# Performance work log

Hardware: AMD Instinct MI355X
Metric: run time of the kernel (lower is better)

Reference implementation:

```python
import jax, jax.numpy as jnp
import numpy as np

EPS = 1e-5  # BatchNorm1d default eps


def gcn_conv(x, row, col, w, n):
    # symmetric normalized aggregation: out[c] = sum_e d[row]^-1/2 d[col]^-1/2 w_e x[row]
    deg = jax.ops.segment_sum(w, col, num_segments=n)           # weighted in-degree [N]
    dinv = jnp.where(deg > 0, jax.lax.rsqrt(deg), 0.0)          # nan_to_num guard
    norm = dinv[row] * dinv[col] * w                            # [E]
    msg = x[row] * norm[:, None]                                # [E, H] gather
    return jax.ops.segment_sum(msg, col, num_segments=n)        # [N, H] scatter-add


def batchnorm(x):
    # BatchNorm1d(affine=False, track_running_stats=False): batch stats, biased var
    mu = jnp.mean(x, axis=0)
    var = jnp.mean((x - mu) ** 2, axis=0)
    return (x - mu) * jax.lax.rsqrt(var + EPS)


def setup_inputs() -> dict:
    key = jax.random.key(0)
    ks = jax.random.split(key, 7)
    N, E, D, H = 100000, 1600000, 128, 128
    x = jax.random.normal(ks[0], (N, D), dtype=jnp.float32)
    edge_index = jax.random.randint(ks[1], (2, E), 0, N, dtype=jnp.int32)
    edge_weight = jax.random.uniform(ks[2], (E,), dtype=jnp.float32)
    # xavier_uniform gain=1: limit = sqrt(6/(fan_in+fan_out))
    lim0 = float(np.sqrt(6.0 / (D + H)))
    lim1 = float(np.sqrt(6.0 / (H + H)))
    W0 = jax.random.uniform(ks[3], (H, D), dtype=jnp.float32, minval=-lim0, maxval=lim0)
    W1 = jax.random.uniform(ks[4], (H, H), dtype=jnp.float32, minval=-lim1, maxval=lim1)
    b0 = jnp.zeros((H,), jnp.float32)
    b1 = jnp.zeros((H,), jnp.float32)
    return {"x": x, "edge_index": edge_index, "edge_weight": edge_weight,
            "W0": W0, "b0": b0, "W1": W1, "b1": b1}


def reference(x, edge_index, edge_weight, W0, b0, W1, b1):
    n = x.shape[0]
    row, col = edge_index[0], edge_index[1]
    # layer 0: linear -> gcn_conv -> bias -> batchnorm -> relu
    h = x @ W0.T
    h = gcn_conv(h, row, col, edge_weight, n)
    h = jax.nn.relu(batchnorm(h + b0))
    # final layer: linear -> gcn_conv -> bias
    h = h @ W1.T
    h = gcn_conv(h, row, col, edge_weight, n)
    return h + b1
```

## Files before the change

### kernel.cpp

```cpp
#include <hip/hip_runtime.h>
#include <cstdint>
#include <cstddef>

#define EPSF 1e-5f
#define BKT 256
#define BKT_SHIFT 8
#define SC_E 4096

typedef unsigned long long ull;
typedef __attribute__((ext_vector_type(8))) short bf16x8;
typedef __attribute__((ext_vector_type(4))) float f32x4;


__global__ __launch_bounds__(512) void bucket_hist(const int* __restrict__ col,
                                                   int* __restrict__ bhist, int E, int NB) {
    __shared__ int lh[512];
    const int t = threadIdx.x;
    lh[t] = 0;
    __syncthreads();
    for (int e = blockIdx.x * 512 + t; e < E; e += gridDim.x * 512)
        atomicAdd(&lh[col[e] >> BKT_SHIFT], 1);
    __syncthreads();
    if (t < NB && lh[t]) atomicAdd(&bhist[t], lh[t]);
}

__global__ __launch_bounds__(512) void scan_buckets(const int* __restrict__ bhist,
                                                    int* __restrict__ bstart,
                                                    int* __restrict__ bcursor,
                                                    int* __restrict__ rs,
                                                    int NB, int N, int E) {
    __shared__ int part[512];
    const int t = threadIdx.x;
    part[t] = (t < NB) ? bhist[t] : 0;
    __syncthreads();
    for (int off = 1; off < 512; off <<= 1) {
        int v = (t >= off) ? part[t - off] : 0;
        __syncthreads();
        part[t] += v;
        __syncthreads();
    }
    int excl = (t == 0) ? 0 : part[t - 1];
    if (t < NB) { bstart[t] = excl; bcursor[t] = excl; }
    if (t == 0) { bstart[NB] = E; rs[N] = E; }
}

__global__ __launch_bounds__(512) void bucket_scatter(const int* __restrict__ row,
                                                      const int* __restrict__ col,
                                                      const float* __restrict__ w,
                                                      int* __restrict__ bcursor,
                                                      int2* __restrict__ brecs,
                                                      int E, int NB) {
    __shared__ int lh[512], lstart[512], lcur[512], gbase[512];
    __shared__ int   sm[SC_E];
    __shared__ float sw[SC_E];
    __shared__ short sb[SC_E];

    const int t = threadIdx.x;
    const int base = blockIdx.x * SC_E;
    const int cnt = min(SC_E, E - base);

    lh[t] = 0;
    __syncthreads();

    int   myb[8], mym[8];
    float myw[8];
#pragma unroll
    for (int k = 0; k < 8; ++k) {
        int i = t + k * 512;
        if (i < cnt) {
            int e = base + i;
            int r = row[e], c = col[e];
            myb[k] = c >> BKT_SHIFT;
            mym[k] = ((c & (BKT - 1)) << 17) | r;
            myw[k] = w[e];
            atomicAdd(&lh[myb[k]], 1);
        } else myb[k] = -1;
    }
    __syncthreads();

    int v = lh[t];
    lstart[t] = v;
    __syncthreads();
    for (int off = 1; off < 512; off <<= 1) {
        int u = (t >= off) ? lstart[t - off] : 0;
        __syncthreads();
        lstart[t] += u;
        __syncthreads();
    }
    int excl = lstart[t] - v;
    __syncthreads();
    lstart[t] = excl;
    lcur[t]   = excl;
    gbase[t]  = (t < NB) ? atomicAdd(&bcursor[t], v) : 0;
    __syncthreads();

#pragma unroll
    for (int k = 0; k < 8; ++k) {
        if (myb[k] >= 0) {
            int slot = atomicAdd(&lcur[myb[k]], 1);
            sm[slot] = mym[k];
            sw[slot] = myw[k];
            sb[slot] = (short)myb[k];
        }
    }
    __syncthreads();

    for (int j = t; j < cnt; j += 512) {
        int b = sb[j];
        int pos = gbase[b] + (j - lstart[b]);
        brecs[pos] = make_int2(sm[j], __float_as_int(sw[j]));
    }
}

__global__ __launch_bounds__(256) void bucket_build(const int2* __restrict__ brecs,
                                                    const int* __restrict__ bstart,
                                                    int* __restrict__ rs,
                                                    float* __restrict__ dinv,
                                                    int2* __restrict__ sedge, int N) {
    __shared__ int   lcnt[256], lscan[256], lcur[256];
    __shared__ float ldeg[256];
    const int b = blockIdx.x, t = threadIdx.x;
    const int s = bstart[b], e = bstart[b + 1];
    const int node0 = b << BKT_SHIFT;
    const int nNodes = min(BKT, N - node0);

    lcnt[t] = 0;
    ldeg[t] = 0.f;
    __syncthreads();

    for (int i = s + t; i < e; i += 256) {
        int2 r = brecs[i];
        int cl = r.x >> 17;
        atomicAdd(&lcnt[cl], 1);
        atomicAdd(&ldeg[cl], __int_as_float(r.y));
    }
    __syncthreads();

    int v = lcnt[t];
    lscan[t] = v;
    __syncthreads();
    for (int off = 1; off < 256; off <<= 1) {
        int u = (t >= off) ? lscan[t - off] : 0;
        __syncthreads();
        lscan[t] += u;
        __syncthreads();
    }
    int excl = lscan[t] - v;
    lcur[t] = excl;
    if (t < nNodes) {
        rs[node0 + t] = s + excl;
        float d = ldeg[t];
        dinv[node0 + t] = (d > 0.f) ? rsqrtf(d) : 0.f;
    }
    __syncthreads();

    for (int i = s + t; i < e; i += 256) {
        int2 r = brecs[i];
        int slot = atomicAdd(&lcur[r.x >> 17], 1);
        sedge[s + slot] = r;
    }
}

__global__ __launch_bounds__(256) void norm_fixup(const int* __restrict__ bstart,
                                                  const float* __restrict__ dinv,
                                                  int2* __restrict__ sedge, int N) {
    __shared__ float ld[256];
    const int b = blockIdx.x, t = threadIdx.x;
    const int node0 = b << BKT_SHIFT;
    const int nNodes = min(BKT, N - node0);
    ld[t] = (t < nNodes) ? dinv[node0 + t] : 0.f;
    const int s = bstart[b], e = bstart[b + 1];
    __syncthreads();
    for (int i = s + t; i < e; i += 256) {
        int2 r = sedge[i];
        int rowi = r.x & 0x1FFFF;
        int cl = r.x >> 17;
        float nrm = dinv[rowi] * ld[cl] * __int_as_float(r.y);
        sedge[i] = make_int2(rowi, __float_as_int(nrm));
    }
}

__device__ __forceinline__ ushort f2bf(float f) {
    uint b = __float_as_uint(f);
    return (ushort)((b + 0x7FFFu + ((b >> 16) & 1u)) >> 16);
}
__device__ __forceinline__ uint4 pack8(const float* f) {
    uint4 o;
    o.x = f2bf(f[0]) | ((uint)f2bf(f[1]) << 16);
    o.y = f2bf(f[2]) | ((uint)f2bf(f[3]) << 16);
    o.z = f2bf(f[4]) | ((uint)f2bf(f[5]) << 16);
    o.w = f2bf(f[6]) | ((uint)f2bf(f[7]) << 16);
    return o;
}

template <bool IN_BF16>
__global__ __launch_bounds__(256) void gemm128_mfma(const void* __restrict__ Xv,
                                                    const float* __restrict__ W,
                                                    ushort* __restrict__ Y, int N) {
    __shared__ __align__(16) ushort Alds[64][128];
    __shared__ __align__(16) ushort Blds[128][128];

    const int t  = threadIdx.x;
    const int n0 = blockIdx.x * 64;

    for (int i = t; i < 128 * 16; i += 256) {
        int j = i >> 4, kc = (i & 15) << 3;
        float f[8];
        *(float4*)&f[0] = *(const float4*)&W[j * 128 + kc];
        *(float4*)&f[4] = *(const float4*)&W[j * 128 + kc + 4];
        *(uint4*)&Blds[j][kc ^ ((j & 7) << 3)] = pack8(f);
    }
    for (int i = t; i < 64 * 16; i += 256) {
        int r = i >> 4, kc = (i & 15) << 3;
        int n = n0 + r;
        uint4 v = make_uint4(0u, 0u, 0u, 0u);
        if (n < N) {
            if constexpr (IN_BF16) {
                v = *(const uint4*)&((const ushort*)Xv)[(size_t)n * 128 + kc];
            } else {
                float f[8];
                *(float4*)&f[0] = *(const float4*)&((const float*)Xv)[(size_t)n * 128 + kc];
                *(float4*)&f[4] = *(const float4*)&((const float*)Xv)[(size_t)n * 128 + kc + 4];
                v = pack8(f);
            }
        }
        *(uint4*)&Alds[r][kc ^ ((r & 7) << 3)] = v;
    }
    __syncthreads();

    const int lane  = t & 63;
    const int wv    = t >> 6;
    const int arow  = wv * 16 + (lane & 15);
    const int klane = (lane >> 4) << 3;
    const int cq    = lane & 15;

    f32x4 acc[8] = {};

    for (int ks = 0; ks < 4; ++ks) {
        const int k0 = ks * 32 + klane;
        bf16x8 a = *(const bf16x8*)&Alds[arow][k0 ^ ((arow & 7) << 3)];
#pragma unroll
        for (int tl = 0; tl < 8; ++tl) {
            int colr = tl * 16 + cq;
            bf16x8 bb = *(const bf16x8*)&Blds[colr][k0 ^ ((colr & 7) << 3)];
            acc[tl] = __builtin_amdgcn_mfma_f32_16x16x32_bf16(a, bb, acc[tl], 0, 0, 0);
        }
    }

    const int r0 = n0 + wv * 16 + ((lane >> 4) << 2);
#pragma unroll
    for (int tl = 0; tl < 8; ++tl) {
#pragma unroll
        for (int reg = 0; reg < 4; ++reg) {
            int rr = r0 + reg;
            if (rr < N) Y[(size_t)rr * 128 + tl * 16 + cq] = f2bf(acc[tl][reg]);
        }
    }
}

__global__ __launch_bounds__(256) void agg_gather(const ushort* __restrict__ Hin,
                                                  const int2* __restrict__ sedge,
                                                  const int* __restrict__ rs,
                                                  const float* __restrict__ bias,
                                                  float* __restrict__ Hout, int N) {
    int c = blockIdx.x * 4 + (threadIdx.x >> 6);
    if (c >= N) return;
    const int lane = threadIdx.x & 63;

    float2 acc;
    if (bias) { acc.x = bias[lane * 2]; acc.y = bias[lane * 2 + 1]; }
    else      { acc.x = 0.f; acc.y = 0.f; }

    int e    = rs[c];
    int eEnd = rs[c + 1];

#define GLOAD(s, nv, vv)                                                       \
    float nv = __int_as_float((s).y);                                         \
    uint  vv = *(const uint*)&Hin[(size_t)(s).x * 128 + lane * 2];

#define GACC(nv, vv)                                                           \
    acc.x = fmaf(nv, __uint_as_float((vv) << 16), acc.x);                      \
    acc.y = fmaf(nv, __uint_as_float((vv) & 0xFFFF0000u), acc.y);

    for (; e + 3 < eEnd; e += 4) {
        int2 s0 = sedge[e], s1 = sedge[e + 1], s2 = sedge[e + 2], s3 = sedge[e + 3];
        GLOAD(s0, n0, v0) GLOAD(s1, n1, v1) GLOAD(s2, n2, v2) GLOAD(s3, n3, v3)
        GACC(n0, v0) GACC(n1, v1) GACC(n2, v2) GACC(n3, v3)
    }
    for (; e < eEnd; ++e) {
        int2 s0 = sedge[e];
        GLOAD(s0, n0, v0)
        GACC(n0, v0)
    }
#undef GLOAD
#undef GACC

    *(float2*)&Hout[(size_t)c * 128 + lane * 2] = acc;
}

__global__ __launch_bounds__(256) void bn_stats(const float* __restrict__ H,
                                                float* __restrict__ sums, int N) {
    int j = threadIdx.x & 127;
    float s = 0.f, s2 = 0.f;
    for (int n = blockIdx.x * 2 + (threadIdx.x >> 7); n < N; n += gridDim.x * 2) {
        float v = H[(size_t)n * 128 + j];
        s += v; s2 += v * v;
    }
    atomicAdd(&sums[j], s);
    atomicAdd(&sums[128 + j], s2);
}

__global__ __launch_bounds__(256) void bn_apply(const float* __restrict__ H,
                                                const float* __restrict__ sums,
                                                ushort* __restrict__ Y, int N, float invN) {
    int idx = blockIdx.x * blockDim.x + threadIdx.x;
    if (idx >= N * 32) return;
    int j0 = (idx & 31) * 4;
    float4 h = *(const float4*)&H[(size_t)idx * 4];
    const float* hv = &h.x;
    ushort o[4];
#pragma unroll
    for (int k = 0; k < 4; ++k) {
        float mu  = sums[j0 + k] * invN;
        float var = sums[128 + j0 + k] * invN - mu * mu;
        float v   = (hv[k] - mu) * rsqrtf(var + EPSF);
        o[k] = f2bf(fmaxf(v, 0.f));
    }
    *(uint2*)&Y[(size_t)idx * 4] =
        make_uint2(o[0] | ((uint)o[1] << 16), o[2] | ((uint)o[3] << 16));
}

extern "C" void kernel_launch(void* const* d_in, const int* in_sizes, int n_in,
                              void* d_out, int out_size, void* d_ws, size_t ws_size,
                              hipStream_t stream) {
    const float* x  = (const float*)d_in[0];
    const int*   ei = (const int*)d_in[1];
    const float* ew = (const float*)d_in[2];
    const float* W0 = (const float*)d_in[3];
    const float* W1 = (const float*)d_in[5];
    const float* b1 = (const float*)d_in[6];

    const int N = in_sizes[0] / 128;
    const int E = in_sizes[2];
    const int* row = ei;
    const int* col = ei + E;
    const int NB = (N + BKT - 1) >> BKT_SHIFT;

    uintptr_t base = (uintptr_t)d_ws;
    auto alloc = [&](size_t bytes) {
        uintptr_t p = base;
        base += (bytes + 255) & ~(size_t)255;
        return (void*)p;
    };
    float*  dinv   = (float*) alloc((size_t)N * 4);
    float*  sums   = (float*) alloc(256 * 4);
    int*    bhist  = (int*)   alloc((size_t)(NB + 1) * 4);
    int*    bstart = (int*)   alloc((size_t)(NB + 1) * 4);
    int*    bcursor= (int*)   alloc((size_t)NB * 4);
    int*    rs     = (int*)   alloc((size_t)(N + 1) * 4);
    int2*   sedge  = (int2*)  alloc((size_t)E * 8);
    ushort* hA     = (ushort*)alloc((size_t)N * 128 * 2);
    ushort* hB     = (ushort*)alloc((size_t)N * 128 * 2);
    int2*   brecs  = (int2*)hB;
    float*  out    = (float*) d_out;
    (void)ws_size; (void)n_in; (void)out_size;

    const float invN = 1.f / (float)N;

    hipMemsetAsync(bhist, 0, (size_t)(NB + 1) * 4, stream);
    hipMemsetAsync(sums, 0, 256 * 4, stream);

    bucket_hist<<<1024, 512, 0, stream>>>(col, bhist, E, NB);
    scan_buckets<<<1, 512, 0, stream>>>(bhist, bstart, bcursor, rs, NB, N, E);
    bucket_scatter<<<(E + SC_E - 1) / SC_E, 512, 0, stream>>>(row, col, ew, bcursor,
                                                              brecs, E, NB);
    bucket_build<<<NB, 256, 0, stream>>>(brecs, bstart, rs, dinv, sedge, N);
    norm_fixup<<<NB, 256, 0, stream>>>(bstart, dinv, sedge, N);

    gemm128_mfma<false><<<(N + 63) / 64, 256, 0, stream>>>(x, W0, hA, N);

    agg_gather<<<(N + 3) / 4, 256, 0, stream>>>(hA, sedge, rs, nullptr, out, N);

    bn_stats<<<512, 256, 0, stream>>>(out, sums, N);
    bn_apply<<<(N * 32 + 255) / 256, 256, 0, stream>>>(out, sums, hB, N, invN);

    gemm128_mfma<true><<<(N + 63) / 64, 256, 0, stream>>>(hB, W1, hA, N);

    agg_gather<<<(N + 3) / 4, 256, 0, stream>>>(hA, sedge, rs, b1, out, N);
}
```

Baseline: 342.4 us.

## Fuse batchnorm apply into second GEMM, store layer-0 aggregation as bf16

```diff
diff --git a/kernel.cpp b/kernel.cpp
--- a/kernel.cpp
+++ b/kernel.cpp
@@ -184,6 +184,9 @@
     uint b = __float_as_uint(f);
     return (ushort)((b + 0x7FFFu + ((b >> 16) & 1u)) >> 16);
 }
+__device__ __forceinline__ float bf2f(ushort u) {
+    return __uint_as_float((uint)u << 16);
+}
 __device__ __forceinline__ uint4 pack8(const float* f) {
     uint4 o;
     o.x = f2bf(f[0]) | ((uint)f2bf(f[1]) << 16);
@@ -193,15 +196,28 @@
     return o;
 }
 
-template <bool IN_BF16>
+template <int MODE>
 __global__ __launch_bounds__(256) void gemm128_mfma(const void* __restrict__ Xv,
                                                     const float* __restrict__ W,
-                                                    ushort* __restrict__ Y, int N) {
+                                                    ushort* __restrict__ Y, int N,
+                                                    const float* __restrict__ sums,
+                                                    float invN) {
     __shared__ __align__(16) ushort Alds[64][128];
     __shared__ __align__(16) ushort Blds[128][128];
+    __shared__ float bnmu[128], bnrs[128];
 
     const int t  = threadIdx.x;
     const int n0 = blockIdx.x * 64;
+
+    if constexpr (MODE == 2) {
+        if (t < 128) {
+            float mu  = sums[t] * invN;
+            float var = sums[128 + t] * invN - mu * mu;
+            bnmu[t] = mu;
+            bnrs[t] = rsqrtf(var + EPSF);
+        }
+        __syncthreads();
+    }
 
     for (int i = t; i < 128 * 16; i += 256) {
         int j = i >> 4, kc = (i & 15) << 3;
@@ -215,12 +231,22 @@
         int n = n0 + r;
         uint4 v = make_uint4(0u, 0u, 0u, 0u);
         if (n < N) {
-            if constexpr (IN_BF16) {
-                v = *(const uint4*)&((const ushort*)Xv)[(size_t)n * 128 + kc];
-            } else {
+            if constexpr (MODE == 0) {
                 float f[8];
                 *(float4*)&f[0] = *(const float4*)&((const float*)Xv)[(size_t)n * 128 + kc];
                 *(float4*)&f[4] = *(const float4*)&((const float*)Xv)[(size_t)n * 128 + kc + 4];
+                v = pack8(f);
+            } else {
+                uint4 raw = *(const uint4*)&((const ushort*)Xv)[(size_t)n * 128 + kc];
+                const uint* rw = &raw.x;
+                float f[8];
+#pragma unroll
+                for (int k = 0; k < 4; ++k) {
+                    float lo = __uint_as_float(rw[k] << 16);
+                    float hi = __uint_as_float(rw[k] & 0xFFFF0000u);
+                    f[2 * k]     = fmaxf((lo - bnmu[kc + 2 * k])     * bnrs[kc + 2 * k],     0.f);
+                    f[2 * k + 1] = fmaxf((hi - bnmu[kc + 2 * k + 1]) * bnrs[kc + 2 * k + 1], 0.f);
+                }
                 v = pack8(f);
             }
         }
@@ -258,11 +284,15 @@
     }
 }
 
+__device__ __forceinline__ float bflo(uint v) { return __uint_as_float(v << 16); }
+__device__ __forceinline__ float bfhi(uint v) { return __uint_as_float(v & 0xFFFF0000u); }
+
+template <bool OUT_BF16>
 __global__ __launch_bounds__(256) void agg_gather(const ushort* __restrict__ Hin,
                                                   const int2* __restrict__ sedge,
                                                   const int* __restrict__ rs,
                                                   const float* __restrict__ bias,
-                                                  float* __restrict__ Hout, int N) {
+                                                  void* __restrict__ Hout, int N, int E) {
     int c = blockIdx.x * 4 + (threadIdx.x >> 6);
     if (c >= N) return;
     const int lane = threadIdx.x & 63;
@@ -271,63 +301,56 @@
     if (bias) { acc.x = bias[lane * 2]; acc.y = bias[lane * 2 + 1]; }
     else      { acc.x = 0.f; acc.y = 0.f; }
 
-    int e    = rs[c];
-    int eEnd = rs[c + 1];
-
-#define GLOAD(s, nv, vv)                                                       \
-    float nv = __int_as_float((s).y);                                         \
-    uint  vv = *(const uint*)&Hin[(size_t)(s).x * 128 + lane * 2];
-
-#define GACC(nv, vv)                                                           \
-    acc.x = fmaf(nv, __uint_as_float((vv) << 16), acc.x);                      \
-    acc.y = fmaf(nv, __uint_as_float((vv) & 0xFFFF0000u), acc.y);
-
-    for (; e + 3 < eEnd; e += 4) {
-        int2 s0 = sedge[e], s1 = sedge[e + 1], s2 = sedge[e + 2], s3 = sedge[e + 3];
-        GLOAD(s0, n0, v0) GLOAD(s1, n1, v1) GLOAD(s2, n2, v2) GLOAD(s3, n3, v3)
-        GACC(n0, v0) GACC(n1, v1) GACC(n2, v2) GACC(n3, v3)
-    }
-    for (; e < eEnd; ++e) {
-        int2 s0 = sedge[e];
-        GLOAD(s0, n0, v0)
-        GACC(n0, v0)
-    }
-#undef GLOAD
-#undef GACC
-
-    *(float2*)&Hout[(size_t)c * 128 + lane * 2] = acc;
-}
-
-__global__ __launch_bounds__(256) void bn_stats(const float* __restrict__ H,
+    const int e0 = rs[c];
+    const int deg = rs[c + 1] - e0;
+
+    for (int base = 0; base < deg; base += 64) {
+        int m = min(64, deg - base);
+        int idx = e0 + base + lane;
+        int2 rec = sedge[idx < E ? idx : E - 1];
+
+        int j = 0;
+        for (; j + 3 < m; j += 4) {
+            int   r0 = __shfl(rec.x, j),     r1 = __shfl(rec.x, j + 1);
+            int   r2 = __shfl(rec.x, j + 2), r3 = __shfl(rec.x, j + 3);
+            float w0 = __int_as_float(__shfl(rec.y, j));
+            float w1 = __int_as_float(__shfl(rec.y, j + 1));
+            float w2 = __int_as_float(__shfl(rec.y, j + 2));
+            float w3 = __int_as_float(__shfl(rec.y, j + 3));
+            uint v0 = *(const uint*)&Hin[(size_t)r0 * 128 + lane * 2];
+            uint v1 = *(const uint*)&Hin[(size_t)r1 * 128 + lane * 2];
+            uint v2 = *(const uint*)&Hin[(size_t)r2 * 128 + lane * 2];
+            uint v3 = *(const uint*)&Hin[(size_t)r3 * 128 + lane * 2];
+            acc.x = fmaf(w0, bflo(v0), acc.x); acc.y = fmaf(w0, bfhi(v0), acc.y);
+            acc.x = fmaf(w1, bflo(v1), acc.x); acc.y = fmaf(w1, bfhi(v1), acc.y);
+            acc.x = fmaf(w2, bflo(v2), acc.x); acc.y = fmaf(w2, bfhi(v2), acc.y);
+            acc.x = fmaf(w3, bflo(v3), acc.x); acc.y = fmaf(w3, bfhi(v3), acc.y);
+        }
+        for (; j < m; ++j) {
+            int   r0 = __shfl(rec.x, j);
+            float w0 = __int_as_float(__shfl(rec.y, j));
+            uint v0 = *(const uint*)&Hin[(size_t)r0 * 128 + lane * 2];
+            acc.x = fmaf(w0, bflo(v0), acc.x); acc.y = fmaf(w0, bfhi(v0), acc.y);
+        }
+    }
+
+    if constexpr (OUT_BF16) {
+        ((uint*)Hout)[(size_t)c * 64 + lane] = f2bf(acc.x) | ((uint)f2bf(acc.y) << 16);
+    } else {
+        *(float2*)&((float*)Hout)[(size_t)c * 128 + lane * 2] = acc;
+    }
+}
+
+__global__ __launch_bounds__(256) void bn_stats(const ushort* __restrict__ H,
                                                 float* __restrict__ sums, int N) {
     int j = threadIdx.x & 127;
     float s = 0.f, s2 = 0.f;
     for (int n = blockIdx.x * 2 + (threadIdx.x >> 7); n < N; n += gridDim.x * 2) {
-        float v = H[(size_t)n * 128 + j];
+        float v = bf2f(H[(size_t)n * 128 + j]);
         s += v; s2 += v * v;
     }
     atomicAdd(&sums[j], s);
     atomicAdd(&sums[128 + j], s2);
-}
-
-__global__ __launch_bounds__(256) void bn_apply(const float* __restrict__ H,
-                                                const float* __restrict__ sums,
-                                                ushort* __restrict__ Y, int N, float invN) {
-    int idx = blockIdx.x * blockDim.x + threadIdx.x;
-    if (idx >= N * 32) return;
-    int j0 = (idx & 31) * 4;
-    float4 h = *(const float4*)&H[(size_t)idx * 4];
-    const float* hv = &h.x;
-    ushort o[4];
-#pragma unroll
-    for (int k = 0; k < 4; ++k) {
-        float mu  = sums[j0 + k] * invN;
-        float var = sums[128 + j0 + k] * invN - mu * mu;
-        float v   = (hv[k] - mu) * rsqrtf(var + EPSF);
-        o[k] = f2bf(fmaxf(v, 0.f));
-    }
-    *(uint2*)&Y[(size_t)idx * 4] =
-        make_uint2(o[0] | ((uint)o[1] << 16), o[2] | ((uint)o[3] << 16));
 }
 
 extern "C" void kernel_launch(void* const* d_in, const int* in_sizes, int n_in,
@@ -377,14 +400,13 @@
     bucket_build<<<NB, 256, 0, stream>>>(brecs, bstart, rs, dinv, sedge, N);
     norm_fixup<<<NB, 256, 0, stream>>>(bstart, dinv, sedge, N);
 
-    gemm128_mfma<false><<<(N + 63) / 64, 256, 0, stream>>>(x, W0, hA, N);
-
-    agg_gather<<<(N + 3) / 4, 256, 0, stream>>>(hA, sedge, rs, nullptr, out, N);
-
-    bn_stats<<<512, 256, 0, stream>>>(out, sums, N);
-    bn_apply<<<(N * 32 + 255) / 256, 256, 0, stream>>>(out, sums, hB, N, invN);
-
-    gemm128_mfma<true><<<(N + 63) / 64, 256, 0, stream>>>(hB, W1, hA, N);
-
-    agg_gather<<<(N + 3) / 4, 256, 0, stream>>>(hA, sedge, rs, b1, out, N);
-}
+    gemm128_mfma<0><<<(N + 63) / 64, 256, 0, stream>>>(x, W0, hA, N, nullptr, 0.f);
+
+    agg_gather<true><<<(N + 3) / 4, 256, 0, stream>>>(hA, sedge, rs, nullptr, hB, N, E);
+
+    bn_stats<<<512, 256, 0, stream>>>(hB, sums, N);
+
+    gemm128_mfma<2><<<(N + 63) / 64, 256, 0, stream>>>(hB, W1, hA, N, sums, invN);
+
+    agg_gather<false><<<(N + 3) / 4, 256, 0, stream>>>(hA, sedge, rs, b1, out, N, E);
+}
```

After: 305.6 us. -10.7%, faster.
